# Kernel tuning notes

Measured on AMD Instinct MI355X. Metric: run time of the kernel, lower is better.

## Reference

```python
import jax, jax.numpy as jnp
import numpy as np

NUM_HEADS = 16
THETA = 10000.0


def _apply_rope(x, pos):
    # x: [b, h, t, d_k], pos: [t] int
    d = x.shape[-1]
    inv_freq = THETA ** (-jnp.arange(0, d, 2, dtype=jnp.float32) / d)  # [d/2]
    ang = pos.astype(jnp.float32)[:, None] * inv_freq                  # [t, d/2]
    cos, sin = jnp.cos(ang), jnp.sin(ang)
    x1, x2 = x[..., ::2], x[..., 1::2]
    r1 = x1 * cos - x2 * sin
    r2 = x1 * sin + x2 * cos
    return jnp.stack([r1, r2], axis=-1).reshape(x.shape)


def setup_inputs() -> dict:
    key = jax.random.key(0)
    k1, k2, k3 = jax.random.split(key, 3)
    b, t, dm = 4, 2048, 2048
    in_features = jax.random.normal(k1, (b, t, dm), dtype=jnp.float32)
    token_positions = jnp.arange(t, dtype=jnp.int64)
    W_qkv = jax.random.normal(k2, (3 * dm, dm), dtype=jnp.float32) * 0.02
    W_o = jax.random.normal(k3, (dm, dm), dtype=jnp.float32) * 0.02
    return {"in_features": in_features, "token_positions": token_positions,
            "W_qkv": W_qkv, "W_o": W_o}


def reference(in_features, token_positions, W_qkv, W_o):
    b, t, dm = in_features.shape
    h = NUM_HEADS
    dk = dm // h
    # fused QKV projection (Linear: y = x W^T)
    qkv = in_features @ W_qkv.T                       # [b, t, 3*dm]
    q, k, v = jnp.split(qkv, 3, axis=-1)
    def to_heads(x):
        return x.reshape(b, t, h, dk).transpose(0, 2, 1, 3)  # [b, h, t, dk]
    q, k, v = to_heads(q), to_heads(k), to_heads(v)
    q = _apply_rope(q, token_positions)
    k = _apply_rope(k, token_positions)
    # causal SDPA
    scale = 1.0 / np.sqrt(dk).astype(np.float32)
    scores = jnp.einsum('bhqd,bhkd->bhqk', q, k) * scale
    causal = jnp.tril(jnp.ones((t, t), dtype=bool))
    scores = jnp.where(causal, scores, jnp.finfo(scores.dtype).min)
    attn = jax.nn.softmax(scores, axis=-1)
    out = jnp.einsum('bhqk,bhkd->bhqd', attn, v)      # [b, h, t, dk]
    out = out.transpose(0, 2, 1, 3).reshape(b, t, dm)
    return out @ W_o.T
```

## Files before the change

### kernel.cpp

```cpp
#include <hip/hip_runtime.h>

typedef unsigned short u16;
typedef __attribute__((ext_vector_type(8))) short s8v;
typedef __attribute__((ext_vector_type(8))) __bf16 bf8;
typedef __attribute__((ext_vector_type(4))) float f4v;

#define GLB(p) ((const __attribute__((address_space(1))) void*)(p))
#define LDS(p) ((__attribute__((address_space(3))) void*)(p))

static __device__ __forceinline__ float b2f(u16 u) {
    union { unsigned int i; float f; } v; v.i = ((unsigned int)u) << 16; return v.f;
}
static __device__ __forceinline__ u16 f2b(float f) {
    union { float f; unsigned int i; } v; v.f = f;
    v.i += 0x7fffu + ((v.i >> 16) & 1u);
    return (u16)(v.i >> 16);
}

__global__ __launch_bounds__(256) void k_conv(const float* __restrict__ in,
                                              u16* __restrict__ out, int n4) {
    int i = blockIdx.x * 256 + threadIdx.x;
    if (i >= n4) return;
    float4 v = ((const float4*)in)[i];
    union { u16 u[4]; unsigned long long ll; } o;
    o.u[0] = f2b(v.x); o.u[1] = f2b(v.y); o.u[2] = f2b(v.z); o.u[3] = f2b(v.w);
    ((unsigned long long*)out)[i] = o.ll;
}

template<int MODE>
__global__ __launch_bounds__(512, 2) void k_gemm_bt(
    const u16* __restrict__ A, const u16* __restrict__ B,
    int K, int N, int gx,
    u16* __restrict__ Qb, u16* __restrict__ Kb, u16* __restrict__ Vt,
    float* __restrict__ Cf)
{
    extern __shared__ __align__(16) u16 Ls[];

    const int t    = threadIdx.x;
    const int lane = t & 63;
    const int wid  = t >> 6;
    const int wm = wid >> 2, wn = wid & 3;
    const int la = lane & 15, lb = lane >> 4;

    const int bid = (int)blockIdx.x;
    const int id2 = (bid & 7) * ((int)gridDim.x >> 3) + (bid >> 3);
    const int bx = id2 % gx, by = id2 / gx;
    const long arow0 = (long)by * 256;
    const long brow0 = (long)bx * 256;

    const int sr = t >> 3;
    const int sg = (t & 7) ^ (sr & 7);
    const u16* Asrc = A + (arow0 + sr) * (long)K + sg * 8;
    const u16* Bsrc = B + (brow0 + sr) * (long)K + sg * 8;
    const long K64 = 64 * (long)K, K128 = 128 * (long)K;
    u16* ldst = Ls + t * 8;

#define STG(q_, op_, h_, kt_) do {                                              \
        const u16* s_ = ((op_) ? Bsrc : Asrc) + (h_) * K128 + (long)(kt_) * 64; \
        u16* d_ = ldst + (q_) * 32768 + (op_) * 16384 + (h_) * 4096 * 2;        \
        __builtin_amdgcn_global_load_lds(GLB(s_),       LDS(d_),        16, 0, 0); \
        __builtin_amdgcn_global_load_lds(GLB(s_ + K64), LDS(d_ + 4096), 16, 0, 0); \
    } while (0)
#define BAR() asm volatile("s_barrier" ::: "memory")
#define VM6() asm volatile("s_waitcnt vmcnt(6)" ::: "memory")
#define RD(off) (*(const bf8*)(Ls + (off)))

    f4v acc[8][4];
#pragma unroll
    for (int m = 0; m < 8; m++)
#pragma unroll
        for (int n = 0; n < 4; n++) acc[m][n] = (f4v){0.f, 0.f, 0.f, 0.f};

    const int r7 = la & 7;
    const int gA0 = (lb ^ r7) * 8;
    const int gA1 = ((lb ^ r7) ^ 4) * 8;
    const int aRow = wm * 8192 + la * 64;
    const int bRow = 16384 + (wn >> 1) * 8192 + ((wn & 1) * 64 + la) * 64;

    const int NKT = K >> 6;
    STG(0, 0, 0, 0); STG(0, 0, 1, 0); STG(0, 1, 0, 0); STG(0, 1, 1, 0);
    asm volatile("s_waitcnt vmcnt(0)\n\ts_barrier" ::: "memory");

    for (int X = 0; X < NKT; ++X) {
        const int D = (X & 1) << 15;
        const int q = (X + 1) & 1;
        const int S = (X + 1 < NKT) ? X + 1 : NKT - 1;
        bf8 aR[4][2], b0[2][2], b1[2][2];

#pragma unroll
        for (int mi = 0; mi < 4; mi++) {
            aR[mi][0] = RD(D + aRow + mi * 1024 + gA0);
            aR[mi][1] = RD(D + aRow + mi * 1024 + gA1);
        }
#pragma unroll
        for (int nl = 0; nl < 2; nl++) {
            b0[nl][0] = RD(D + bRow + nl * 1024 + gA0);
            b0[nl][1] = RD(D + bRow + nl * 1024 + gA1);
        }
        STG(q, 0, 0, S); STG(q, 0, 1, S); STG(q, 1, 0, S); STG(q, 1, 1, S);
        BAR();
        __builtin_amdgcn_s_setprio(1);
#pragma unroll
        for (int mi = 0; mi < 4; mi++)
#pragma unroll
            for (int nl = 0; nl < 2; nl++) {
                acc[mi][nl] = __builtin_amdgcn_mfma_f32_16x16x32_bf16(aR[mi][0], b0[nl][0], acc[mi][nl], 0, 0, 0);
                acc[mi][nl] = __builtin_amdgcn_mfma_f32_16x16x32_bf16(aR[mi][1], b0[nl][1], acc[mi][nl], 0, 0, 0);
            }
        __builtin_amdgcn_s_setprio(0);
        BAR();

#pragma unroll
        for (int nl = 0; nl < 2; nl++) {
            b1[nl][0] = RD(D + bRow + (2 + nl) * 1024 + gA0);
            b1[nl][1] = RD(D + bRow + (2 + nl) * 1024 + gA1);
        }
        BAR();
        __builtin_amdgcn_s_setprio(1);
#pragma unroll
        for (int mi = 0; mi < 4; mi++)
#pragma unroll
            for (int nl = 0; nl < 2; nl++) {
                acc[mi][2 + nl] = __builtin_amdgcn_mfma_f32_16x16x32_bf16(aR[mi][0], b1[nl][0], acc[mi][2 + nl], 0, 0, 0);
                acc[mi][2 + nl] = __builtin_amdgcn_mfma_f32_16x16x32_bf16(aR[mi][1], b1[nl][1], acc[mi][2 + nl], 0, 0, 0);
            }
        __builtin_amdgcn_s_setprio(0);
        BAR();

#pragma unroll
        for (int mi = 0; mi < 4; mi++) {
            aR[mi][0] = RD(D + aRow + (4 + mi) * 1024 + gA0);
            aR[mi][1] = RD(D + aRow + (4 + mi) * 1024 + gA1);
        }
        BAR();
        __builtin_amdgcn_s_setprio(1);
#pragma unroll
        for (int mi = 0; mi < 4; mi++)
#pragma unroll
            for (int nl = 0; nl < 2; nl++) {
                acc[4 + mi][2 + nl] = __builtin_amdgcn_mfma_f32_16x16x32_bf16(aR[mi][0], b1[nl][0], acc[4 + mi][2 + nl], 0, 0, 0);
                acc[4 + mi][2 + nl] = __builtin_amdgcn_mfma_f32_16x16x32_bf16(aR[mi][1], b1[nl][1], acc[4 + mi][2 + nl], 0, 0, 0);
            }
        __builtin_amdgcn_s_setprio(0);
        BAR();

        VM6();
        BAR();
        __builtin_amdgcn_s_setprio(1);
#pragma unroll
        for (int mi = 0; mi < 4; mi++)
#pragma unroll
            for (int nl = 0; nl < 2; nl++) {
                acc[4 + mi][nl] = __builtin_amdgcn_mfma_f32_16x16x32_bf16(aR[mi][0], b0[nl][0], acc[4 + mi][nl], 0, 0, 0);
                acc[4 + mi][nl] = __builtin_amdgcn_mfma_f32_16x16x32_bf16(aR[mi][1], b0[nl][1], acc[4 + mi][nl], 0, 0, 0);
            }
        __builtin_amdgcn_s_setprio(0);
        BAR();
    }
    asm volatile("s_waitcnt vmcnt(0)" ::: "memory");
#undef STG
#undef BAR
#undef VM6
#undef RD

#pragma unroll
    for (int mi = 0; mi < 8; mi++) {
#pragma unroll
        for (int ni = 0; ni < 4; ni++) {
            const long grow0 = arow0 + wm * 128 + mi * 16 + lb * 4;
            const int  gcol  = (int)brow0 + wn * 64 + ni * 16 + la;
#pragma unroll
            for (int i = 0; i < 4; i++) {
                const float v = acc[mi][ni][i];
                const long r = grow0 + i;
                if (MODE == 0) {
                    const int part = gcol >> 11;
                    const int rem  = gcol & 2047;
                    const int head = rem >> 7, d = rem & 127;
                    const long bh = (r >> 11) * 16 + head;
                    const int tt = (int)(r & 2047);
                    if (part == 2) {
                        Vt[(bh << 18) + ((long)d << 11) + tt] = f2b(v);
                    } else {
                        u16* dst = (part == 0) ? Qb : Kb;
                        dst[((bh << 11) + tt) * 128 + d] = f2b(v);
                    }
                } else {
                    Cf[r * (long)N + gcol] = v;
                }
            }
        }
    }
}

__global__ __launch_bounds__(256) void k_rope(u16* __restrict__ Qb, u16* __restrict__ Kb,
                                              const int* __restrict__ pos) {
    const int idx = blockIdx.x * 256 + threadIdx.x;
    const int j  = idx & 63;
    const int t  = (idx >> 6) & 2047;
    const int bh = (idx >> 17) & 63;
    u16* P = (idx >> 23) ? Kb : Qb;
    const long off = ((((long)bh << 11) + t) << 7) + 2 * j;
    unsigned int raw = *(unsigned int*)(P + off);
    float x1 = b2f((u16)(raw & 0xffffu));
    float x2 = b2f((u16)(raw >> 16));
    float invf = exp2f((float)j * -0.20762050593046014f);
    float ang = (float)pos[t] * invf;
    float sn, cs;
    sincosf(ang, &sn, &cs);
    unsigned int o = (unsigned int)f2b(x1 * cs - x2 * sn)
                   | ((unsigned int)f2b(x1 * sn + x2 * cs) << 16);
    *(unsigned int*)(P + off) = o;
}

__global__ __launch_bounds__(512) void k_attn(const u16* __restrict__ Qb,
                                              const u16* __restrict__ Kb,
                                              const u16* __restrict__ Vt,
                                              u16* __restrict__ Ob)
{
    __shared__ __align__(16) u16 Ks[2][32 * 128];
    __shared__ __align__(16) u16 Vs[2][64 * 64];
    __shared__ __align__(16) u16 Pl[8][32 * 32];

    const int tid  = threadIdx.x;
    const int lane = tid & 63;
    const int w    = tid >> 6;
    const int la = lane & 15, lb = lane >> 4;
    const int qg = 7 - ((int)blockIdx.x >> 6);
    const int bh = blockIdx.x & 63;
    const long base = (long)bh << 18;
    const int qt = qg * 8 + w;
    const int q0 = qt * 32;
    const int tiles_w = qt + 1;
    const int NT = qg * 8 + 8;
    const float scale = 0.08838834764831845f;

    bf8 qf[2][4];
#pragma unroll
    for (int m = 0; m < 2; m++)
#pragma unroll
        for (int kb = 0; kb < 4; kb++)
            qf[m][kb] = *(const bf8*)(Qb + base + (long)(q0 + m * 16 + la) * 128 + kb * 32 + lb * 8);

    f4v o[2][8];
#pragma unroll
    for (int m = 0; m < 2; m++)
#pragma unroll
        for (int n = 0; n < 8; n++) o[m][n] = (f4v){0.f, 0.f, 0.f, 0.f};
    float lst[2][4];
#pragma unroll
    for (int m = 0; m < 2; m++)
#pragma unroll
        for (int i = 0; i < 4; i++) lst[m][i] = 0.f;

    char* Pb = (char*)(Pl[w]);

    const int ko = tid * 16;
    const int kr = ko >> 8, kc = (ko & 255) ^ ((kr & 7) << 4);
    const int vo = tid * 16;
    const int vR = vo >> 7, vc = (vo & 127) ^ ((vR & 7) << 4);
    const int vd = 2 * vR + (vc >> 6), vt = (vc & 63) >> 1;

#define STAGE(buf, jt_) do {                                                        \
        const int kv0_ = (jt_) * 32;                                               \
        __builtin_amdgcn_global_load_lds(                                          \
            GLB(Kb + base + (long)(kv0_ + kr) * 128 + (kc >> 1)),                  \
            LDS((u16*)Ks[buf] + tid * 8), 16, 0, 0);                               \
        __builtin_amdgcn_global_load_lds(                                          \
            GLB(Vt + base + ((long)vd << 11) + kv0_ + vt),                         \
            LDS((u16*)Vs[buf] + tid * 8), 16, 0, 0);                               \
    } while (0)

    STAGE(0, 0);

    for (int jt = 0; jt < NT; ++jt) {
        const int buf = jt & 1;
        __syncthreads();
        if (jt + 1 < NT) STAGE(buf ^ 1, jt + 1);

        if (jt < tiles_w) {
            const char* KsB = (const char*)Ks[buf];
            const char* VsB = (const char*)Vs[buf];

            f4v s[2][2];
            s[0][0] = s[0][1] = s[1][0] = s[1][1] = (f4v){0.f, 0.f, 0.f, 0.f};
#pragma unroll
            for (int n = 0; n < 2; n++) {
                const int row = n * 16 + la;
#pragma unroll
                for (int kb = 0; kb < 4; kb++) {
                    bf8 kf = *(const bf8*)(KsB + row * 256 + ((kb * 64 + lb * 16) ^ ((row & 7) << 4)));
                    s[0][n] = __builtin_amdgcn_mfma_f32_16x16x32_bf16(qf[0][kb], kf, s[0][n], 0, 0, 0);
                    s[1][n] = __builtin_amdgcn_mfma_f32_16x16x32_bf16(qf[1][kb], kf, s[1][n], 0, 0, 0);
                }
            }

            bf8 vf[8];
#pragma unroll
            for (int nO = 0; nO < 8; nO++) {
                const int R = nO * 8 + (la >> 1);
                vf[nO] = *(const bf8*)(VsB + R * 128 + (((la & 1) * 64 + lb * 16) ^ ((R & 7) << 4)));
            }

            const bool diag = (jt == qt);
            float p[2][2][4];
#pragma unroll
            for (int m = 0; m < 2; m++)
#pragma unroll
                for (int n = 0; n < 2; n++)
#pragma unroll
                    for (int i = 0; i < 4; i++) {
                        float v = __expf(fmaf(s[m][n][i], scale, -8.0f));
                        if (diag && (n * 16 + la) > (m * 16 + lb * 4 + i)) v = 0.f;
                        p[m][n][i] = v;
                        lst[m][i] += v;
                    }

#pragma unroll
            for (int m = 0; m < 2; m++)
#pragma unroll
                for (int n = 0; n < 2; n++)
#pragma unroll
                    for (int i = 0; i < 4; i++) {
                        const int row = m * 16 + lb * 4 + i;
                        const int colb = (n * 16 + la) * 2;
                        *(u16*)(Pb + row * 64 + (colb ^ ((row & 3) << 4))) = f2b(p[m][n][i]);
                    }
            bf8 pa[2];
#pragma unroll
            for (int am = 0; am < 2; am++) {
                const int row = am * 16 + la;
                pa[am] = *(const bf8*)(Pb + row * 64 + ((lb * 16) ^ ((row & 3) << 4)));
            }
#pragma unroll
            for (int nO = 0; nO < 8; nO++) {
                o[0][nO] = __builtin_amdgcn_mfma_f32_16x16x32_bf16(pa[0], vf[nO], o[0][nO], 0, 0, 0);
                o[1][nO] = __builtin_amdgcn_mfma_f32_16x16x32_bf16(pa[1], vf[nO], o[1][nO], 0, 0, 0);
            }
        }
        __syncthreads();
    }
#undef STAGE

    float linv[2][4];
#pragma unroll
    for (int m = 0; m < 2; m++)
#pragma unroll
        for (int i = 0; i < 4; i++) {
            float l = lst[m][i];
            l += __shfl_xor(l, 1);
            l += __shfl_xor(l, 2);
            l += __shfl_xor(l, 4);
            l += __shfl_xor(l, 8);
            linv[m][i] = 1.0f / l;
        }

    const int b = bh >> 4, h = bh & 15;
#pragma unroll
    for (int m = 0; m < 2; m++)
#pragma unroll
        for (int nO = 0; nO < 8; nO++)
#pragma unroll
            for (int i = 0; i < 4; i++) {
                const int row = q0 + m * 16 + lb * 4 + i;
                const int d = nO * 16 + la;
                Ob[((long)(b * 2048 + row) << 11) + h * 128 + d] = f2b(o[m][nO][i] * linv[m][i]);
            }
}

extern "C" void kernel_launch(void* const* d_in, const int* in_sizes, int n_in,
                              void* d_out, int out_size, void* d_ws, size_t ws_size,
                              hipStream_t stream)
{
    const float* X    = (const float*)d_in[0];
    const int*   pos  = (const int*)d_in[1];
    const float* Wqkv = (const float*)d_in[2];
    const float* Wo   = (const float*)d_in[3];
    float* out = (float*)d_out;

    char* ws = (char*)d_ws;
    u16* Xb    = (u16*)(ws + 0);
    u16* Wqkvb = (u16*)(ws + 33554432);
    u16* Wob   = (u16*)(ws + 58720256);
    u16* Qb    = (u16*)(ws + 67108864);
    u16* Kb    = (u16*)(ws + 100663296);
    u16* Vt    = (u16*)(ws + 134217728);
    u16* Ob    = (u16*)(ws + 167772160);

    k_conv<<<16384, 256, 0, stream>>>(X, Xb, 4194304);
    k_conv<<<12288, 256, 0, stream>>>(Wqkv, Wqkvb, 3145728);
    k_conv<<<4096, 256, 0, stream>>>(Wo, Wob, 1048576);
    k_gemm_bt<0><<<768, 512, 131072, stream>>>(Xb, Wqkvb, 2048, 6144, 24, Qb, Kb, Vt, nullptr);
    k_rope<<<65536, 256, 0, stream>>>(Qb, Kb, pos);
    k_attn<<<512, 512, 0, stream>>>(Qb, Kb, Vt, Ob);
    k_gemm_bt<1><<<256, 512, 131072, stream>>>(Ob, Wob, 2048, 2048, 8, nullptr, nullptr, nullptr, out);
}
```

Baseline: 486.7 us.

## Stage QKV GEMM epilogue through LDS for coalesced vector stores and trim barriers

The QKV GEMM epilogue now writes its accumulator tile into LDS and then issues coalesced 16-byte stores to Q, K and the transposed V layout, replacing scattered 2-byte global stores. The main loop drops half of its barriers and replaces the partial vmcnt(6) wait with a full vmcnt(0) before the last MFMA block. Dynamic LDS grows to hold the padded staging tile, which may lower occupancy. The full wait may also shorten the overlap between loads and compute.

Result: faster. 436.2 us (-10.4%).

```diff
diff --git a/kernel.cpp b/kernel.cpp
--- a/kernel.cpp
+++ b/kernel.cpp
@@ -57,12 +57,10 @@
 
 #define STG(q_, op_, h_, kt_) do {                                              \
         const u16* s_ = ((op_) ? Bsrc : Asrc) + (h_) * K128 + (long)(kt_) * 64; \
-        u16* d_ = ldst + (q_) * 32768 + (op_) * 16384 + (h_) * 4096 * 2;        \
+        u16* d_ = ldst + (q_) * 32768 + (op_) * 16384 + (h_) * 8192;            \
         __builtin_amdgcn_global_load_lds(GLB(s_),       LDS(d_),        16, 0, 0); \
         __builtin_amdgcn_global_load_lds(GLB(s_ + K64), LDS(d_ + 4096), 16, 0, 0); \
     } while (0)
-#define BAR() asm volatile("s_barrier" ::: "memory")
-#define VM6() asm volatile("s_waitcnt vmcnt(6)" ::: "memory")
 #define RD(off) (*(const bf8*)(Ls + (off)))
 
     f4v acc[8][4];
@@ -79,7 +77,8 @@
 
     const int NKT = K >> 6;
     STG(0, 0, 0, 0); STG(0, 0, 1, 0); STG(0, 1, 0, 0); STG(0, 1, 1, 0);
-    asm volatile("s_waitcnt vmcnt(0)\n\ts_barrier" ::: "memory");
+    asm volatile("s_waitcnt vmcnt(0)" ::: "memory");
+    __builtin_amdgcn_s_barrier();
 
     for (int X = 0; X < NKT; ++X) {
         const int D = (X & 1) << 15;
@@ -98,7 +97,7 @@
             b0[nl][1] = RD(D + bRow + nl * 1024 + gA1);
         }
         STG(q, 0, 0, S); STG(q, 0, 1, S); STG(q, 1, 0, S); STG(q, 1, 1, S);
-        BAR();
+        __builtin_amdgcn_s_barrier();
         __builtin_amdgcn_s_setprio(1);
 #pragma unroll
         for (int mi = 0; mi < 4; mi++)
@@ -108,14 +107,13 @@
                 acc[mi][nl] = __builtin_amdgcn_mfma_f32_16x16x32_bf16(aR[mi][1], b0[nl][1], acc[mi][nl], 0, 0, 0);
             }
         __builtin_amdgcn_s_setprio(0);
-        BAR();
 
 #pragma unroll
         for (int nl = 0; nl < 2; nl++) {
             b1[nl][0] = RD(D + bRow + (2 + nl) * 1024 + gA0);
             b1[nl][1] = RD(D + bRow + (2 + nl) * 1024 + gA1);
         }
-        BAR();
+        __builtin_amdgcn_s_barrier();
         __builtin_amdgcn_s_setprio(1);
 #pragma unroll
         for (int mi = 0; mi < 4; mi++)
@@ -125,14 +123,13 @@
                 acc[mi][2 + nl] = __builtin_amdgcn_mfma_f32_16x16x32_bf16(aR[mi][1], b1[nl][1], acc[mi][2 + nl], 0, 0, 0);
             }
         __builtin_amdgcn_s_setprio(0);
-        BAR();
 
 #pragma unroll
         for (int mi = 0; mi < 4; mi++) {
             aR[mi][0] = RD(D + aRow + (4 + mi) * 1024 + gA0);
             aR[mi][1] = RD(D + aRow + (4 + mi) * 1024 + gA1);
         }
-        BAR();
+        __builtin_amdgcn_s_barrier();
         __builtin_amdgcn_s_setprio(1);
 #pragma unroll
         for (int mi = 0; mi < 4; mi++)
@@ -142,10 +139,9 @@
                 acc[4 + mi][2 + nl] = __builtin_amdgcn_mfma_f32_16x16x32_bf16(aR[mi][1], b1[nl][1], acc[4 + mi][2 + nl], 0, 0, 0);
             }
         __builtin_amdgcn_s_setprio(0);
-        BAR();
-
-        VM6();
-        BAR();
+
+        asm volatile("s_waitcnt vmcnt(0)" ::: "memory");
+        __builtin_amdgcn_s_barrier();
         __builtin_amdgcn_s_setprio(1);
 #pragma unroll
         for (int mi = 0; mi < 4; mi++)
@@ -155,40 +151,75 @@
                 acc[4 + mi][nl] = __builtin_amdgcn_mfma_f32_16x16x32_bf16(aR[mi][1], b0[nl][1], acc[4 + mi][nl], 0, 0, 0);
             }
         __builtin_amdgcn_s_setprio(0);
-        BAR();
     }
-    asm volatile("s_waitcnt vmcnt(0)" ::: "memory");
 #undef STG
-#undef BAR
-#undef VM6
 #undef RD
 
-#pragma unroll
-    for (int mi = 0; mi < 8; mi++) {
-#pragma unroll
-        for (int ni = 0; ni < 4; ni++) {
-            const long grow0 = arow0 + wm * 128 + mi * 16 + lb * 4;
-            const int  gcol  = (int)brow0 + wn * 64 + ni * 16 + la;
-#pragma unroll
-            for (int i = 0; i < 4; i++) {
-                const float v = acc[mi][ni][i];
-                const long r = grow0 + i;
-                if (MODE == 0) {
-                    const int part = gcol >> 11;
-                    const int rem  = gcol & 2047;
-                    const int head = rem >> 7, d = rem & 127;
-                    const long bh = (r >> 11) * 16 + head;
-                    const int tt = (int)(r & 2047);
-                    if (part == 2) {
-                        Vt[(bh << 18) + ((long)d << 11) + tt] = f2b(v);
-                    } else {
-                        u16* dst = (part == 0) ? Qb : Kb;
-                        dst[((bh << 11) + tt) * 128 + d] = f2b(v);
-                    }
-                } else {
-                    Cf[r * (long)N + gcol] = v;
+    if (MODE == 1) {
+#pragma unroll
+        for (int mi = 0; mi < 8; mi++)
+#pragma unroll
+            for (int ni = 0; ni < 4; ni++) {
+                const long grow0 = arow0 + wm * 128 + mi * 16 + lb * 4;
+                const int  gcol  = (int)brow0 + wn * 64 + ni * 16 + la;
+#pragma unroll
+                for (int i = 0; i < 4; i++)
+                    Cf[(grow0 + i) * (long)N + gcol] = acc[mi][ni][i];
+            }
+        return;
+    }
+
+    __syncthreads();
+    const int part = (int)(brow0 >> 11);
+    const int colp = (int)brow0 & 2047;
+    const int h0   = colp >> 7;
+    const int bidx = (int)(arow0 >> 11);
+    const int t0   = (int)arow0 & 2047;
+
+    if (part == 2) {
+#pragma unroll
+        for (int mi = 0; mi < 8; mi++)
+#pragma unroll
+            for (int ni = 0; ni < 4; ni++) {
+                const int tlb = wm * 128 + mi * 16 + lb * 4;
+                const int dl  = wn * 64 + ni * 16 + la;
+#pragma unroll
+                for (int i2 = 0; i2 < 2; i2++) {
+                    unsigned int pk = (unsigned int)f2b(acc[mi][ni][i2 * 2])
+                                    | ((unsigned int)f2b(acc[mi][ni][i2 * 2 + 1]) << 16);
+                    *(unsigned int*)(Ls + dl * 264 + tlb + i2 * 2) = pk;
                 }
             }
+        __syncthreads();
+        const int w = wid;
+#pragma unroll
+        for (int j = 0; j < 16; j++) {
+            const int dl = j * 16 + w * 2 + (lane >> 5);
+            const int c  = lane & 31;
+            bf8 v = *(const bf8*)(Ls + dl * 264 + c * 8);
+            const long bh = (long)(bidx * 16 + h0 + (dl >> 7));
+            *(bf8*)(Vt + (bh << 18) + ((long)(dl & 127) << 11) + t0 + c * 8) = v;
+        }
+    } else {
+        u16* dst = (part == 0) ? Qb : Kb;
+#pragma unroll
+        for (int mi = 0; mi < 8; mi++)
+#pragma unroll
+            for (int ni = 0; ni < 4; ni++) {
+                const int tlb = wm * 128 + mi * 16 + lb * 4;
+                const int dl  = wn * 64 + ni * 16 + la;
+#pragma unroll
+                for (int i = 0; i < 4; i++)
+                    Ls[(tlb + i) * 264 + dl] = f2b(acc[mi][ni][i]);
+            }
+        __syncthreads();
+#pragma unroll
+        for (int j = 0; j < 16; j++) {
+            const int R  = j * 32 + (t >> 4);
+            const int tl = R >> 1, hh = R & 1, c = t & 15;
+            bf8 v = *(const bf8*)(Ls + tl * 264 + hh * 128 + c * 8);
+            const long bh = (long)(bidx * 16 + h0 + hh);
+            *(bf8*)(dst + ((bh << 11) + t0 + tl) * 128 + c * 8) = v;
         }
     }
 }
@@ -390,8 +421,8 @@
     k_conv<<<16384, 256, 0, stream>>>(X, Xb, 4194304);
     k_conv<<<12288, 256, 0, stream>>>(Wqkv, Wqkvb, 3145728);
     k_conv<<<4096, 256, 0, stream>>>(Wo, Wob, 1048576);
-    k_gemm_bt<0><<<768, 512, 131072, stream>>>(Xb, Wqkvb, 2048, 6144, 24, Qb, Kb, Vt, nullptr);
+    k_gemm_bt<0><<<768, 512, 139392, stream>>>(Xb, Wqkvb, 2048, 6144, 24, Qb, Kb, Vt, nullptr);
     k_rope<<<65536, 256, 0, stream>>>(Qb, Kb, pos);
     k_attn<<<512, 512, 0, stream>>>(Qb, Kb, Vt, Ob);
-    k_gemm_bt<1><<<256, 512, 131072, stream>>>(Ob, Wob, 2048, 2048, 8, nullptr, nullptr, nullptr, out);
-}
+    k_gemm_bt<1><<<256, 512, 139392, stream>>>(Ob, Wob, 2048, 2048, 8, nullptr, nullptr, nullptr, out);
+}
```
